# Kernel tuning notes

Hardware: AMD Instinct MI355X
Metric: run time of the kernel (lower is better)

Reference implementation:

```python
import jax, jax.numpy as jnp
import numpy as np

B, D, N, S = 1024, 512, 500000, 32768


def setup_inputs() -> dict:
    key = jax.random.key(0)
    k1, k2, k3 = jax.random.split(key, 3)
    inputs = jax.random.normal(k1, (B, D), dtype=jnp.float32)
    # Linear(D, N) init: uniform(-0.05, 0.05) weight, zero bias
    weight = jax.random.uniform(k2, (N, D), dtype=jnp.float32, minval=-0.05, maxval=0.05)
    bias = jnp.zeros((N,), dtype=jnp.float32)
    sample_ids = jax.random.randint(k3, (S,), 0, N, dtype=jnp.int64)
    return {"inputs": inputs, "weight": weight, "bias": bias, "sample_ids": sample_ids}


def reference(inputs, weight, bias, sample_ids):
    # Gather retrieved class embeddings: [S, D] and their biases [S]
    sample_weights = weight[sample_ids]
    sample_bias = bias[sample_ids]
    # Sampled logits: inputs @ sample_weights.T + bias  -> [B, S]
    # (matches sample_weights.matmul(inputs.t()).t() + sample_bias in torch)
    logits = jnp.einsum("bd,sd->bs", inputs, sample_weights) + sample_bias
    return logits
```

## Files before the change

### kernel.cpp

```cpp
#include <hip/hip_runtime.h>
#include <stdint.h>

#define B_DIM 1024
#define D_DIM 512
#define S_DIM 32768

typedef __attribute__((ext_vector_type(8))) short bf16x8;
typedef __attribute__((ext_vector_type(4))) float f32x4;
typedef __attribute__((ext_vector_type(8))) unsigned short u16x8;

#define AS1 __attribute__((address_space(1)))
#define AS3 __attribute__((address_space(3)))

__device__ __forceinline__ unsigned short f2bf(float f) {
  union { float f; uint32_t u; } x; x.f = f;
  uint32_t r = x.u + 0x7fffu + ((x.u >> 16) & 1u);
  return (unsigned short)(r >> 16);
}
__device__ __forceinline__ uint32_t cvtpk(float a, float b) {
  uint32_t r;
  asm("v_cvt_pk_bf16_f32 %0, %1, %2" : "=v"(r) : "v"(a), "v"(b));
  return r;
}

__global__ __launch_bounds__(256) void conv_a(const float* __restrict__ A,
                                              unsigned short* __restrict__ Ab) {
  int gid = blockIdx.x * 256 + threadIdx.x;
  const float* src = A + (size_t)gid * 8;
  float4 v0 = *(const float4*)src;
  float4 v1 = *(const float4*)(src + 4);
  u16x8 o;
  o[0] = f2bf(v0.x); o[1] = f2bf(v0.y); o[2] = f2bf(v0.z); o[3] = f2bf(v0.w);
  o[4] = f2bf(v1.x); o[5] = f2bf(v1.y); o[6] = f2bf(v1.z); o[7] = f2bf(v1.w);
  *(u16x8*)(Ab + (size_t)gid * 8) = o;
}

#define BN 128
#define NG 64
#define B_OFF 32768

__global__ __launch_bounds__(512, 2) void gemm_fused(const unsigned short* __restrict__ Ab,
                                                     const float* __restrict__ W,
                                                     const float* __restrict__ bias,
                                                     const int* __restrict__ ids,
                                                     float* __restrict__ out) {
  __shared__ __attribute__((aligned(16))) char lds[163840];

  const int tid = threadIdx.x;
  const int lane = tid & 63;
  const int w = tid >> 6;
  const int wm = w >> 1;
  const int wn = w & 1;
  const int lq = lane >> 4;
  const int l16 = lane & 15;
  const int n0 = blockIdx.x * BN;

  const char* srcA[2];
#pragma unroll
  for (int j = 0; j < 2; ++j) {
    const int p = j * 512 + tid;
    const int line = p >> 3;
    const int sl = (p & 7) ^ (line & 7);
    const int row = line * 2 + (sl >> 2);
    srcA[j] = (const char*)Ab + row * 1024 + (sl & 3) * 16;
  }
  auto stage = [&](int g) {
    const int off = (g >> 4) * 262144 + (g & 15) * 64;
    char* dst = lds + (g & 1) * 16384 + w * 1024;
#pragma unroll
    for (int j = 0; j < 2; ++j)
      __builtin_amdgcn_global_load_lds((const AS1 void*)(srcA[j] + off),
                                       (AS3 void*)(dst + j * 8192), 16, 0, 0);
  };

  stage(0);

  {
    const int row = tid >> 2;
    const int c = tid & 3;
    const int myid = ids[n0 + row];
    const float* srcW = W + (size_t)myid * D_DIM;
    char* drow = lds + B_OFF + row * 1024;
    const int r7 = row & 7;
#pragma unroll
    for (int j = 0; j < 16; ++j) {
      const float* p = srcW + j * 32 + c * 8;
      float4 a = *(const float4*)p;
      float4 b = *(const float4*)(p + 4);
      int4 o;
      o.x = cvtpk(a.x, a.y); o.y = cvtpk(a.z, a.w);
      o.z = cvtpk(b.x, b.y); o.w = cvtpk(b.z, b.w);
      const int slot = (c + j * 4) ^ r7;
      *(int4*)(drow + slot * 16) = o;
    }
  }
  float bb[4];
#pragma unroll
  for (int n = 0; n < 4; ++n)
    bb[n] = bias[ids[n0 + wn * 64 + n * 16 + l16]];

  __syncthreads();

  int aoff[4];
#pragma unroll
  for (int m = 0; m < 4; ++m) {
    const int row = wm * 64 + m * 16 + l16;
    const int s = (((row & 1) << 2) | lq) ^ ((row >> 1) & 7);
    aoff[m] = (row >> 1) * 128 + s * 16;
  }
  int bbase[4], bx7[4];
#pragma unroll
  for (int n = 0; n < 4; ++n) {
    const int col = wn * 64 + n * 16 + l16;
    bbase[n] = B_OFF + col * 1024;
    bx7[n] = col & 7;
  }

  f32x4 acc[4][4];
#pragma unroll
  for (int m = 0; m < 4; ++m)
#pragma unroll
    for (int n = 0; n < 4; ++n)
      acc[m][n] = (f32x4)0.0f;

  for (int g = 0; g < NG; ++g) {
    __builtin_amdgcn_sched_barrier(0);
    if (g < NG - 1) {
      stage(g + 1);
      __builtin_amdgcn_sched_barrier(0);
      asm volatile("s_waitcnt vmcnt(2)" ::: "memory");
    } else {
      asm volatile("s_waitcnt vmcnt(0)" ::: "memory");
    }
    __builtin_amdgcn_s_barrier();
    __builtin_amdgcn_sched_barrier(0);

    const char* bufa = lds + (g & 1) * 16384;
    const int kt4 = (g & 15) << 2;

    bf16x8 af[4], bv[4];
#pragma unroll
    for (int m = 0; m < 4; ++m)
      af[m] = *(const bf16x8*)(bufa + aoff[m]);
#pragma unroll
    for (int n = 0; n < 4; ++n)
      bv[n] = *(const bf16x8*)(lds + bbase[n] + (((kt4 + lq) ^ bx7[n]) << 4));

    __builtin_amdgcn_s_setprio(1);
#pragma unroll
    for (int m = 0; m < 4; ++m)
#pragma unroll
      for (int n = 0; n < 4; ++n)
        acc[m][n] = __builtin_amdgcn_mfma_f32_16x16x32_bf16(af[m], bv[n],
                                                            acc[m][n], 0, 0, 0);
    __builtin_amdgcn_s_setprio(0);

    __builtin_amdgcn_sched_barrier(0);
    __builtin_amdgcn_s_barrier();

    if ((g & 15) == 15) {
      const int rt = (g >> 4) * 256 + wm * 64 + lq * 4;
#pragma unroll
      for (int n = 0; n < 4; ++n) {
        const int col = n0 + wn * 64 + n * 16 + l16;
#pragma unroll
        for (int m = 0; m < 4; ++m) {
          const int rbase = rt + m * 16;
#pragma unroll
          for (int r = 0; r < 4; ++r)
            out[(size_t)(rbase + r) * S_DIM + col] = acc[m][n][r] + bb[n];
          acc[m][n] = (f32x4)0.0f;
        }
      }
    }
  }
}

extern "C" void kernel_launch(void* const* d_in, const int* in_sizes, int n_in,
                              void* d_out, int out_size, void* d_ws, size_t ws_size,
                              hipStream_t stream) {
  const float* inp  = (const float*)d_in[0];
  const float* W    = (const float*)d_in[1];
  const float* bias = (const float*)d_in[2];
  const int*   ids  = (const int*)d_in[3];
  float* out = (float*)d_out;

  unsigned short* Ab = (unsigned short*)d_ws;

  conv_a<<<(B_DIM * D_DIM / 8) / 256, 256, 0, stream>>>(inp, Ab);

  dim3 grid(S_DIM / BN);
  gemm_fused<<<grid, 512, 0, stream>>>(Ab, W, bias, ids, out);
}
```

Before: 68.07 us.

## Software-pipeline LDS fragment reads and spread output stores across K iterations

Restructures the main loop so the LDS fragments for the next K tile are read into a second register set while the current tile's MFMAs run. Global-to-LDS staging is issued two tiles ahead instead of one. Finished row-block accumulators are copied into a second accumulator array and written out in chunks over the next eight iterations, rather than as one burst of stores that stalls the loop. This adds register pressure (double fragments and a second 4x4 accumulator set) and relies on hand-tuned vmcnt and lgkmcnt waits, which risks spills or lower occupancy.

```diff
diff --git a/kernel.cpp b/kernel.cpp
--- a/kernel.cpp
+++ b/kernel.cpp
@@ -115,64 +115,96 @@
     bbase[n] = B_OFF + col * 1024;
     bx7[n] = col & 7;
   }
-
-  f32x4 acc[4][4];
+  const int c0 = n0 + wn * 64 + l16;
+
+  auto readf = [&](bf16x8 (&af)[4], bf16x8 (&bv)[4], int tile, int par) {
+    const char* bufa = lds + par * 16384;
+    const int kslot = (tile & 15) << 2;
+#pragma unroll
+    for (int m = 0; m < 4; ++m) af[m] = *(const bf16x8*)(bufa + aoff[m]);
+#pragma unroll
+    for (int n = 0; n < 4; ++n)
+      bv[n] = *(const bf16x8*)(lds + bbase[n] + (((kslot + lq) ^ bx7[n]) << 4));
+  };
+
+  f32x4 acc[4][4], acc2[4][4];
 #pragma unroll
   for (int m = 0; m < 4; ++m)
 #pragma unroll
-    for (int n = 0; n < 4; ++n)
-      acc[m][n] = (f32x4)0.0f;
-
-  for (int g = 0; g < NG; ++g) {
-    __builtin_amdgcn_sched_barrier(0);
-    if (g < NG - 1) {
-      stage(g + 1);
-      __builtin_amdgcn_sched_barrier(0);
-      asm volatile("s_waitcnt vmcnt(2)" ::: "memory");
-    } else {
-      asm volatile("s_waitcnt vmcnt(0)" ::: "memory");
+    for (int n = 0; n < 4; ++n) { acc[m][n] = (f32x4)0.0f; acc2[m][n] = (f32x4)0.0f; }
+
+  bf16x8 afA[4], bvA[4], afB[4], bvB[4];
+
+  stage(1);
+  readf(afA, bvA, 0, 0);
+
+  int rt2 = wm * 64 + lq * 4;
+
+  auto body = [&](int g, int par, bf16x8 (&cAf)[4], bf16x8 (&cBv)[4],
+                  bf16x8 (&nAf)[4], bf16x8 (&nBv)[4]) {
+    const int gm = g & 15;
+    const bool spread = (g >= 17) && (gm >= 1) && (gm <= 8);
+    if (spread) asm volatile("s_waitcnt vmcnt(8)" ::: "memory");
+    else        asm volatile("s_waitcnt vmcnt(0)" ::: "memory");
+    __builtin_amdgcn_s_barrier();
+    __builtin_amdgcn_sched_barrier(0);
+    if (g < NG - 1) readf(nAf, nBv, g + 1, par ^ 1);
+    __builtin_amdgcn_sched_barrier(0);
+    asm volatile("s_waitcnt lgkmcnt(8)" ::: "memory");
+    __builtin_amdgcn_sched_barrier(0);
+    __builtin_amdgcn_s_barrier();
+    if (g < NG - 2) stage(g + 2);
+    __builtin_amdgcn_sched_barrier(0);
+    if (g >= 16 && gm <= 7) {
+      const int jn = gm >> 1;
+      const int ms = (gm & 1) << 1;
+      const int cc = c0 + jn * 16;
+      const int rb = ((g >> 4) - 1) * 256 + rt2;
+#pragma unroll
+      for (int t = 0; t < 2; ++t) {
+        const int m = ms + t;
+#pragma unroll
+        for (int r = 0; r < 4; ++r)
+          out[(size_t)(rb + m * 16 + r) * S_DIM + cc] = acc2[m][jn][r] + bb[jn];
+      }
     }
-    __builtin_amdgcn_s_barrier();
-    __builtin_amdgcn_sched_barrier(0);
-
-    const char* bufa = lds + (g & 1) * 16384;
-    const int kt4 = (g & 15) << 2;
-
-    bf16x8 af[4], bv[4];
+    __builtin_amdgcn_sched_barrier(0);
+    __builtin_amdgcn_s_setprio(1);
 #pragma unroll
     for (int m = 0; m < 4; ++m)
-      af[m] = *(const bf16x8*)(bufa + aoff[m]);
-#pragma unroll
-    for (int n = 0; n < 4; ++n)
-      bv[n] = *(const bf16x8*)(lds + bbase[n] + (((kt4 + lq) ^ bx7[n]) << 4));
-
-    __builtin_amdgcn_s_setprio(1);
-#pragma unroll
-    for (int m = 0; m < 4; ++m)
 #pragma unroll
       for (int n = 0; n < 4; ++n)
-        acc[m][n] = __builtin_amdgcn_mfma_f32_16x16x32_bf16(af[m], bv[n],
+        acc[m][n] = __builtin_amdgcn_mfma_f32_16x16x32_bf16(cAf[m], cBv[n],
                                                             acc[m][n], 0, 0, 0);
     __builtin_amdgcn_s_setprio(0);
-
-    __builtin_amdgcn_sched_barrier(0);
-    __builtin_amdgcn_s_barrier();
-
-    if ((g & 15) == 15) {
-      const int rt = (g >> 4) * 256 + wm * 64 + lq * 4;
-#pragma unroll
-      for (int n = 0; n < 4; ++n) {
-        const int col = n0 + wn * 64 + n * 16 + l16;
-#pragma unroll
-        for (int m = 0; m < 4; ++m) {
-          const int rbase = rt + m * 16;
-#pragma unroll
-          for (int r = 0; r < 4; ++r)
-            out[(size_t)(rbase + r) * S_DIM + col] = acc[m][n][r] + bb[n];
-          acc[m][n] = (f32x4)0.0f;
+    __builtin_amdgcn_sched_barrier(0);
+    if (gm == 15) {
+      if (g == NG - 1) {
+        const int rb = 3 * 256 + rt2;
+#pragma unroll
+        for (int n = 0; n < 4; ++n) {
+          const int cc = c0 + n * 16;
+#pragma unroll
+          for (int m = 0; m < 4; ++m)
+#pragma unroll
+            for (int r = 0; r < 4; ++r)
+              out[(size_t)(rb + m * 16 + r) * S_DIM + cc] = acc[m][n][r] + bb[n];
         }
+      } else {
+#pragma unroll
+        for (int m = 0; m < 4; ++m)
+#pragma unroll
+          for (int n = 0; n < 4; ++n) {
+            acc2[m][n] = acc[m][n];
+            acc[m][n] = (f32x4)0.0f;
+          }
       }
     }
+  };
+
+  for (int g = 0; g < NG; g += 2) {
+    body(g,     0, afA, bvA, afB, bvB);
+    body(g + 1, 1, afB, bvB, afA, bvA);
   }
 }
 
```

After: 113.6 us. +66.9%, slower.
